# Optimization experiments

Measured on AMD Instinct MI355X. Metric: run time of the kernel, lower is better.

Reference implementation:

```python
import jax, jax.numpy as jnp
import numpy as np
import math

B = 256          # batch size
D = 128          # input_size (embed dim)
N = 500000       # output_size == num_samples (memory bank rows)
K = 2048         # num_negative_samples
T = 0.07         # temperature
MOM = 0.5        # momentum
EPS = 1e-07


def _l2norm(x):
    return x / jnp.linalg.norm(x, axis=-1, keepdims=True)


def setup_inputs() -> dict:
    key = jax.random.key(0)
    k1, k2, k3, k4, k5, k6 = jax.random.split(key, 6)
    stdv = 1.0 / math.sqrt(D / 3.0)
    memory_v1 = jax.random.uniform(k1, (N, D), dtype=jnp.float32) * (2 * stdv) - stdv
    memory_v2 = jax.random.uniform(k2, (N, D), dtype=jnp.float32) * (2 * stdv) - stdv
    # embeds come out of an L2-normalization module in the original pipeline
    student_embed = _l2norm(jax.random.normal(k3, (B, D), dtype=jnp.float32))
    teacher_embed = _l2norm(jax.random.normal(k4, (B, D), dtype=jnp.float32))
    pos_idx = jax.random.randint(k5, (B,), 0, N, dtype=jnp.int64)
    contrast_idx = jax.random.randint(k6, (B, K + 1), 0, N, dtype=jnp.int64)
    contrast_idx = contrast_idx.at[:, 0].set(pos_idx)  # column 0 holds the positive
    return {
        'student_embed': student_embed,
        'teacher_embed': teacher_embed,
        'memory_v1': memory_v1,
        'memory_v2': memory_v2,
        'pos_idx': pos_idx,
        'contrast_idx': contrast_idx,
    }


def _contrast_loss(x):
    # x: [B, K+1] normalized exp-similarities; column 0 is the positive
    m = x.shape[1] - 1
    pn = 1.0 / float(N)  # num_samples
    noise = m * pn + EPS
    p_pos = x[:, 0]
    log_d1 = jnp.log(p_pos / (p_pos + noise))
    p_neg = x[:, 1:]
    log_d0 = jnp.log((m * pn) / (p_neg + noise))
    return -(log_d1.sum() + log_d0.sum()) / x.shape[0]


def reference(student_embed, teacher_embed, memory_v1, memory_v2, pos_idx, contrast_idx):
    output_size = memory_v1.shape[0]
    # gather [B, K+1, D] rows from each bank (detached in original)
    w1 = jax.lax.stop_gradient(memory_v1[contrast_idx])
    w2 = jax.lax.stop_gradient(memory_v2[contrast_idx])
    # per-sample bmm + exp/div  (teacher scored against v1 bank, student against v2)
    out_v2 = jnp.exp(jnp.einsum('bkd,bd->bk', w1, teacher_embed) / T)
    out_v1 = jnp.exp(jnp.einsum('bkd,bd->bk', w2, student_embed) / T)
    # first-call normalization constants (treated as constants thereafter)
    z_v1 = jax.lax.stop_gradient(out_v1.mean() * output_size)
    z_v2 = jax.lax.stop_gradient(out_v2.mean() * output_size)
    out_v1 = out_v1 / z_v1
    out_v2 = out_v2 / z_v2
    # momentum-weighted renormalize-and-scatter memory update (no_grad)
    s = jax.lax.stop_gradient(student_embed)
    t = jax.lax.stop_gradient(teacher_embed)
    l_pos = memory_v1[pos_idx] * MOM + s * (1.0 - MOM)
    updated_v1 = l_pos / jnp.sqrt((l_pos ** 2).sum(1, keepdims=True))
    new_memory_v1 = memory_v1.at[pos_idx].set(updated_v1)
    ab_pos = memory_v2[pos_idx] * MOM + t * (1.0 - MOM)
    updated_v2 = ab_pos / jnp.sqrt((ab_pos ** 2).sum(1, keepdims=True))
    new_memory_v2 = memory_v2.at[pos_idx].set(updated_v2)
    loss = _contrast_loss(out_v1) + _contrast_loss(out_v2)
    return loss, new_memory_v1, new_memory_v2
```

## Files before the change

kernel.cpp:

```cpp
#include <hip/hip_runtime.h>
#include <math.h>

namespace {
constexpr int kB = 256;
constexpr int kD = 128;
constexpr int kN = 500000;
constexpr int kKC = 2049;
constexpr int kNPair = kB * kKC;
constexpr float kTInv = 1.0f / 0.07f;
constexpr float kMom = 0.5f;
constexpr int kRB = 256;
constexpr long long kM = (long long)kN * kD;
constexpr long long kTot = 2 * kM;
constexpr int kChunk = 2048;
constexpr int kNB1 = (kN + kChunk - 1) / kChunk;
constexpr int kRows = 32;
constexpr int kTPB = kN / kRows;
constexpr int kTiles = 2 * kTPB;
constexpr int kLdsStride = 132;
constexpr int kTilesPerBlock = 16;
constexpr int kGrid9 = (kTiles + kTilesPerBlock - 1) / kTilesPerBlock;

typedef float fx4 __attribute__((ext_vector_type(4)));
}


__global__ __launch_bounds__(256) void hist_kernel(const int* __restrict__ cidx, int* __restrict__ A)
{
    int i = blockIdx.x * 256 + threadIdx.x;
    if (i < kNPair) atomicAdd(&A[cidx[i]], 1);
}

__global__ __launch_bounds__(256) void scan1_kernel(const int* __restrict__ A, int* __restrict__ bsum)
{
    long long base = (long long)blockIdx.x * kChunk;
    int t = threadIdx.x;
    int s = 0;
    #pragma unroll
    for (int j = 0; j < 8; ++j) {
        long long i = base + t * 8 + j;
        if (i < kN) s += A[i];
    }
    __shared__ int lds[256];
    lds[t] = s; __syncthreads();
    for (int st = 128; st > 0; st >>= 1) {
        if (t < st) lds[t] += lds[t + st];
        __syncthreads();
    }
    if (t == 0) bsum[blockIdx.x] = lds[0];
}

__global__ __launch_bounds__(256) void scan2_kernel(
    const int* __restrict__ bsum, int* __restrict__ bpre, int* __restrict__ offs)
{
    int t = threadIdx.x;
    int v = (t < kNB1) ? bsum[t] : 0;
    __shared__ int lds[256];
    lds[t] = v; __syncthreads();
    for (int st = 1; st < 256; st <<= 1) {
        int add = (t >= st) ? lds[t - st] : 0;
        __syncthreads();
        lds[t] += add;
        __syncthreads();
    }
    if (t < kNB1) bpre[t] = lds[t] - v;
    if (t == kNB1 - 1) offs[kN] = lds[t];
}

__global__ __launch_bounds__(256) void scan3_kernel(
    const int* __restrict__ A, const int* __restrict__ bpre, int* __restrict__ offs)
{
    int t = threadIdx.x;
    long long base = (long long)blockIdx.x * kChunk;
    int c[8]; int s = 0;
    #pragma unroll
    for (int j = 0; j < 8; ++j) {
        long long i = base + t * 8 + j;
        c[j] = (i < kN) ? A[i] : 0;
        s += c[j];
    }
    __shared__ int lds[256];
    lds[t] = s; __syncthreads();
    for (int st = 1; st < 256; st <<= 1) {
        int add = (t >= st) ? lds[t - st] : 0;
        __syncthreads();
        lds[t] += add;
        __syncthreads();
    }
    int excl = lds[t] - s + bpre[blockIdx.x];
    #pragma unroll
    for (int j = 0; j < 8; ++j) {
        long long i = base + t * 8 + j;
        if (i < kN) { offs[i] = excl; excl += c[j]; }
    }
}

__global__ __launch_bounds__(256) void scatter_kernel(
    const int* __restrict__ cidx, const int* __restrict__ offs,
    int* __restrict__ cur, long long* __restrict__ sorted64)
{
    int p = blockIdx.x * 256 + threadIdx.x;
    if (p < kNPair) {
        int r = cidx[p];
        int pos = offs[r] + atomicAdd(&cur[r], 1);
        sorted64[pos] = ((long long)r << 20) | (long long)p;
    }
}

__global__ __launch_bounds__(256) void fused9_kernel(
    const float* __restrict__ mem1, const float* __restrict__ mem2,
    const float* __restrict__ teacher, const float* __restrict__ student,
    const int* __restrict__ offs, const long long* __restrict__ sorted64,
    float* __restrict__ out, float* __restrict__ e2, float* __restrict__ e1)
{
    __shared__ float tile[kRows * kLdsStride];
    __shared__ long long s64lds[2][256];
    const int tid = threadIdx.x;
    const int lane = tid & 63;
    const int w = tid >> 6;
    fx4* ov = reinterpret_cast<fx4*>(out);

    if (blockIdx.x == 0 && tid == 0)
        __builtin_nontemporal_store(mem2[kM - 1], &out[kTot]);

    const int T0 = blockIdx.x * kTilesPerBlock;
    int T1 = T0 + kTilesPerBlock; if (T1 > kTiles) T1 = kTiles;
    const int nT = T1 - T0;

    auto r0of = [](int T) { return (T >= kTPB) ? (T - kTPB) * kRows : T * kRows; };

    int rA = r0of(T0);
    int oA = offs[rA];
    int cA = offs[rA + kRows] - oA;
    int TBn = (1 < nT) ? T0 + 1 : T0;
    int rB = r0of(TBn);
    int oB = offs[rB];
    int cB = (1 < nT) ? (offs[rB + kRows] - oB) : 0;
    {
        long long v = 0;
        if (tid < cA) v = sorted64[oA + tid];
        s64lds[0][tid] = v;
    }
    float4 sl0, sl1, sl2, sl3;
    float carry;
    {
        int bk = (T0 >= kTPB);
        const float4* bank4 = reinterpret_cast<const float4*>(bk ? mem2 : mem1);
        long long lb4 = (long long)(bk ? T0 - kTPB : T0) * (kRows * kD / 4) + w * 256;
        sl0 = bank4[lb4 + 0 * 64 + lane];
        sl1 = bank4[lb4 + 1 * 64 + lane];
        sl2 = bank4[lb4 + 2 * 64 + lane];
        sl3 = bank4[lb4 + 3 * 64 + lane];
        long long gb = (long long)bk * kM + (long long)rA * kD + (long long)w * 1024;
        carry = 0.f;
        if (gb > 0) { long long g2 = gb - 1; carry = (g2 < kM) ? mem1[g2] : mem2[g2 - kM]; }
    }

    for (int i = 0; i < nT; ++i) {
        const int T = T0 + i;
        const int cur = i & 1;
        const int bk = (T >= kTPB) ? 1 : 0;
        const int r0 = r0of(T);
        const int o0 = oA, cnt = cA;

        float4 sn0, sn1, sn2, sn3;
        float carryn;
        {
            int Tn = (i + 1 < nT) ? T + 1 : T;
            int bkn = (Tn >= kTPB);
            const float4* bank4 = reinterpret_cast<const float4*>(bkn ? mem2 : mem1);
            long long lb4 = (long long)(bkn ? Tn - kTPB : Tn) * (kRows * kD / 4) + w * 256;
            sn0 = bank4[lb4 + 0 * 64 + lane];
            sn1 = bank4[lb4 + 1 * 64 + lane];
            sn2 = bank4[lb4 + 2 * 64 + lane];
            sn3 = bank4[lb4 + 3 * 64 + lane];
            long long gb = (long long)bkn * kM + (long long)r0of(Tn) * kD + (long long)w * 1024;
            carryn = 0.f;
            if (gb > 0) { long long g2 = gb - 1; carryn = (g2 < kM) ? mem1[g2] : mem2[g2 - kM]; }
        }
        long long s64n = 0;
        if (tid < cB) s64n = sorted64[oB + tid];
        int oC, cC;
        {
            int Tn2 = (i + 2 < nT) ? T + 2 : T;
            int rn2 = r0of(Tn2);
            oC = offs[rn2];
            cC = (i + 2 < nT) ? (offs[rn2 + kRows] - oC) : 0;
        }
        __builtin_amdgcn_sched_barrier(0);

        {
            const long long gbase = (long long)bk * kM + (long long)r0 * kD
                                    + (long long)w * 1024;
            const long long g4 = gbase >> 2;
            float cr = carry;
            float4 v[4] = {sl0, sl1, sl2, sl3};
            #pragma unroll
            for (int i2 = 0; i2 < 4; ++i2) {
                float4 c = v[i2];
                int lr = w * 8 + i2 * 2 + (lane >> 5);
                *reinterpret_cast<float4*>(&tile[lr * kLdsStride + (lane & 31) * 4]) = c;
                float pw = __shfl_up(c.w, 1);
                if (lane == 0) pw = cr;
                cr = __shfl(c.w, 63);
                long long k4 = g4 + i2 * 64 + lane;
                if (k4 != 0) {
                    fx4 st = {pw, c.x, c.y, c.z};
                    __builtin_nontemporal_store(st, &ov[k4]);
                } else {
                    __builtin_nontemporal_store(c.x, &out[1]);
                    __builtin_nontemporal_store(c.y, &out[2]);
                    __builtin_nontemporal_store(c.z, &out[3]);
                }
            }
        }
        asm volatile("s_waitcnt lgkmcnt(0)" ::: "memory");
        __builtin_amdgcn_sched_barrier(0);
        __builtin_amdgcn_s_barrier();
        __builtin_amdgcn_sched_barrier(0);

        {
            s64lds[cur ^ 1][tid] = s64n;

            const float4* emb4 = reinterpret_cast<const float4*>(bk ? student : teacher);
            float* ep = bk ? e1 : e2;
            const int sub = tid & 3;
            for (int t = tid >> 2; t < cnt; t += 64) {
                long long v = (t < 256) ? s64lds[cur][t] : sorted64[o0 + t];
                int p  = (int)(v & 0xFFFFF);
                int lr = (int)(v >> 20) - r0;
                const float4* er = emb4
                    + (long long)((unsigned)p / (unsigned)kKC) * 32 + sub * 8;
                const float* row = &tile[lr * kLdsStride + sub * 32];
                float ax = 0.f, ay = 0.f, az = 0.f, aw = 0.f;
                #pragma unroll
                for (int kk = 0; kk < 8; ++kk) {
                    int c4 = (kk + sub * 2) & 7;
                    float4 ev = er[c4];
                    float4 rv = *reinterpret_cast<const float4*>(&row[c4 * 4]);
                    ax += rv.x * ev.x; ay += rv.y * ev.y;
                    az += rv.z * ev.z; aw += rv.w * ev.w;
                }
                float d = (ax + ay) + (az + aw);
                d += __shfl_xor(d, 1);
                d += __shfl_xor(d, 2);
                if (sub == 0) ep[p] = __expf(d * kTInv);
            }
        }
        __builtin_amdgcn_sched_barrier(0);
        asm volatile("s_waitcnt lgkmcnt(0)" ::: "memory");
        __builtin_amdgcn_s_barrier();
        __builtin_amdgcn_sched_barrier(0);

        sl0 = sn0; sl1 = sn1; sl2 = sn2; sl3 = sn3;
        carry = carryn;
        oA = oB; cA = cB; oB = oC; cB = cC;
    }
}


__global__ __launch_bounds__(256) void dots_kernel(
    const float* __restrict__ mem1, const float* __restrict__ mem2,
    const float* __restrict__ teacher, const float* __restrict__ student,
    const int* __restrict__ cidx,
    float* __restrict__ e2, float* __restrict__ e1)
{
    int gtid = blockIdx.x * 256 + threadIdx.x;
    int wave = gtid >> 6;
    int lane = threadIdx.x & 63;
    if (wave >= kNPair) return;
    int b = wave / kKC;
    long long row = (long long)cidx[wave] * kD;
    const float2 m1 = *reinterpret_cast<const float2*>(mem1 + row + lane * 2);
    const float2 m2 = *reinterpret_cast<const float2*>(mem2 + row + lane * 2);
    const float2 tv = *reinterpret_cast<const float2*>(teacher + b * kD + lane * 2);
    const float2 sv = *reinterpret_cast<const float2*>(student + b * kD + lane * 2);
    float d1 = m1.x * tv.x + m1.y * tv.y;
    float d2 = m2.x * sv.x + m2.y * sv.y;
    #pragma unroll
    for (int off = 32; off > 0; off >>= 1) {
        d1 += __shfl_xor(d1, off);
        d2 += __shfl_xor(d2, off);
    }
    if (lane == 0) {
        e2[wave] = __expf(d1 * kTInv);
        e1[wave] = __expf(d2 * kTInv);
    }
}

__global__ __launch_bounds__(256) void copy_kernel(
    const float* __restrict__ mem1, const float* __restrict__ mem2,
    float* __restrict__ out)
{
    const long long NV4 = (kTot + 1) / 4;
    const long long KS  = kM / 4;
    const float4* m1v = reinterpret_cast<const float4*>(mem1);
    const float4* m2v = reinterpret_cast<const float4*>(mem2);
    float4* ov = reinterpret_cast<float4*>(out);
    long long stride = (long long)gridDim.x * 256;
    for (long long k = (long long)blockIdx.x * 256 + threadIdx.x; k < NV4; k += stride) {
        if (k == 0) {
            out[1] = mem1[0]; out[2] = mem1[1]; out[3] = mem1[2];
            out[kTot] = mem2[kM - 1];
            continue;
        }
        float4 r;
        if (k < KS) {
            float4 a = m1v[k - 1];
            float4 b = m1v[k];
            r = make_float4(a.w, b.x, b.y, b.z);
        } else if (k == KS) {
            r = make_float4(mem1[kM - 1], mem2[0], mem2[1], mem2[2]);
        } else {
            float4 a = m2v[k - KS - 1];
            float4 b = m2v[k - KS];
            r = make_float4(a.w, b.x, b.y, b.z);
        }
        ov[k] = r;
    }
}


__global__ __launch_bounds__(256) void sums_kernel(
    const float* __restrict__ e2, const float* __restrict__ e1,
    float* __restrict__ p2, float* __restrict__ p1)
{
    __shared__ float s2[256], s1[256];
    float a2 = 0.f, a1 = 0.f;
    for (int i = blockIdx.x * 256 + threadIdx.x; i < kNPair; i += 256 * kRB) {
        a2 += e2[i];
        a1 += e1[i];
    }
    s2[threadIdx.x] = a2; s1[threadIdx.x] = a1;
    __syncthreads();
    for (int st = 128; st > 0; st >>= 1) {
        if ((int)threadIdx.x < st) {
            s2[threadIdx.x] += s2[threadIdx.x + st];
            s1[threadIdx.x] += s1[threadIdx.x + st];
        }
        __syncthreads();
    }
    if (threadIdx.x == 0) { p2[blockIdx.x] = s2[0]; p1[blockIdx.x] = s1[0]; }
}

__global__ __launch_bounds__(256) void lossp_kernel(
    const float* __restrict__ e2, const float* __restrict__ e1,
    const float* __restrict__ p2, const float* __restrict__ p1,
    float* __restrict__ lp)
{
    __shared__ float s2[256], s1[256];
    s2[threadIdx.x] = p2[threadIdx.x];
    s1[threadIdx.x] = p1[threadIdx.x];
    __syncthreads();
    for (int st = 128; st > 0; st >>= 1) {
        if ((int)threadIdx.x < st) {
            s2[threadIdx.x] += s2[threadIdx.x + st];
            s1[threadIdx.x] += s1[threadIdx.x + st];
        }
        __syncthreads();
    }
    const float scale = (float)kN / (float)kNPair;
    const float iz2 = 1.0f / (s2[0] * scale);
    const float iz1 = 1.0f / (s1[0] * scale);

    const float mpn = 2048.0f / 500000.0f;
    const float noise = mpn + 1e-7f;
    float acc = 0.f;
    for (int i = blockIdx.x * 256 + threadIdx.x; i < kNPair; i += 256 * kRB) {
        int k = i % kKC;
        float x2 = e2[i] * iz2;
        float x1 = e1[i] * iz1;
        if (k == 0) {
            acc += __logf(x2 / (x2 + noise)) + __logf(x1 / (x1 + noise));
        } else {
            acc += __logf(mpn / (x2 + noise)) + __logf(mpn / (x1 + noise));
        }
    }
    __syncthreads();
    __shared__ float s[256];
    s[threadIdx.x] = acc;
    __syncthreads();
    for (int st = 128; st > 0; st >>= 1) {
        if ((int)threadIdx.x < st) s[threadIdx.x] += s[threadIdx.x + st];
        __syncthreads();
    }
    if (threadIdx.x == 0) lp[blockIdx.x] = s[0];
}

__global__ __launch_bounds__(256) void final_kernel(
    const float* __restrict__ lp, float* __restrict__ out)
{
    __shared__ float s[256];
    s[threadIdx.x] = lp[threadIdx.x];
    __syncthreads();
    for (int st = 128; st > 0; st >>= 1) {
        if ((int)threadIdx.x < st) s[threadIdx.x] += s[threadIdx.x + st];
        __syncthreads();
    }
    if (threadIdx.x == 0) out[0] = -s[0] / (float)kB;
}


__global__ __launch_bounds__(64) void update_kernel(
    const float* __restrict__ mem1, const float* __restrict__ mem2,
    const float* __restrict__ student, const float* __restrict__ teacher,
    const int* __restrict__ pos_idx,
    float* __restrict__ out1, float* __restrict__ out2)
{
    int b = blockIdx.x;
    int lane = threadIdx.x;
    int p = pos_idx[b];
    for (int b2 = b + 1; b2 < kB; ++b2)
        if (pos_idx[b2] == p) return;
    long long row = (long long)p * kD;
    float2 m1 = *reinterpret_cast<const float2*>(mem1 + row + lane * 2);
    float2 m2 = *reinterpret_cast<const float2*>(mem2 + row + lane * 2);
    float2 sv = *reinterpret_cast<const float2*>(student + b * kD + lane * 2);
    float2 tv = *reinterpret_cast<const float2*>(teacher + b * kD + lane * 2);
    float2 l1 = make_float2(m1.x * kMom + sv.x * (1.f - kMom),
                            m1.y * kMom + sv.y * (1.f - kMom));
    float2 l2 = make_float2(m2.x * kMom + tv.x * (1.f - kMom),
                            m2.y * kMom + tv.y * (1.f - kMom));
    float n1 = l1.x * l1.x + l1.y * l1.y;
    float n2 = l2.x * l2.x + l2.y * l2.y;
    #pragma unroll
    for (int off = 32; off > 0; off >>= 1) {
        n1 += __shfl_xor(n1, off);
        n2 += __shfl_xor(n2, off);
    }
    float i1 = 1.0f / sqrtf(n1);
    float i2 = 1.0f / sqrtf(n2);
    out1[row + lane * 2]     = l1.x * i1;
    out1[row + lane * 2 + 1] = l1.y * i1;
    out2[row + lane * 2]     = l2.x * i2;
    out2[row + lane * 2 + 1] = l2.y * i2;
}

extern "C" void kernel_launch(void* const* d_in, const int* in_sizes, int n_in,
                              void* d_out, int out_size, void* d_ws, size_t ws_size,
                              hipStream_t stream) {
    const float* student = (const float*)d_in[0];
    const float* teacher = (const float*)d_in[1];
    const float* mem1    = (const float*)d_in[2];
    const float* mem2    = (const float*)d_in[3];
    const int*   pos_idx = (const int*)d_in[4];
    const int*   cidx    = (const int*)d_in[5];

    float* out  = (float*)d_out;
    float* out1 = out + 1;
    float* out2 = out + 1 + kM;

    float* ws = (float*)d_ws;
    float* e2 = ws;
    float* e1 = e2 + kNPair;
    long long* sorted64 = (long long*)(e1 + kNPair);
    float* p2 = (float*)(sorted64 + kNPair);
    float* p1 = p2 + kRB;
    float* lp = p1 + kRB;
    int*   A    = (int*)(lp + kRB);
    int*   cur  = A + kN;
    int*   offs = cur + kN;
    int*   bsum = offs + kN + 1;
    int*   bpre = bsum + kNB1;
    size_t need = (size_t)((char*)(bpre + kNB1) - (char*)d_ws);

    if (ws_size >= need) {
        (void)hipMemsetAsync(A, 0, 2 * (size_t)kN * sizeof(int), stream);
        hist_kernel<<<(kNPair + 255) / 256, 256, 0, stream>>>(cidx, A);
        scan1_kernel<<<kNB1, 256, 0, stream>>>(A, bsum);
        scan2_kernel<<<1, 256, 0, stream>>>(bsum, bpre, offs);
        scan3_kernel<<<kNB1, 256, 0, stream>>>(A, bpre, offs);
        scatter_kernel<<<(kNPair + 255) / 256, 256, 0, stream>>>(cidx, offs, cur, sorted64);
        fused9_kernel<<<kGrid9, 256, 0, stream>>>(mem1, mem2, teacher, student,
                                                  offs, sorted64, out, e2, e1);
    } else {
        int nblocks = (kNPair + 3) / 4;
        dots_kernel<<<nblocks, 256, 0, stream>>>(mem1, mem2, teacher, student, cidx, e2, e1);
        copy_kernel<<<2048, 256, 0, stream>>>(mem1, mem2, out);
    }

    sums_kernel<<<kRB, 256, 0, stream>>>(e2, e1, p2, p1);
    lossp_kernel<<<kRB, 256, 0, stream>>>(e2, e1, p2, p1, lp);
    final_kernel<<<1, 256, 0, stream>>>(lp, out);
    update_kernel<<<kB, 64, 0, stream>>>(mem1, mem2, student, teacher, pos_idx, out1, out2);
}
```

Baseline: 309.1 us.

## Fuse exp-sum reduction into fused gather kernel and halve tiles per block

Each fused9 block now accumulates the exp-similarities it produces and writes per-block partial sums, so the separate sums pass that re-read both e arrays is removed. lossp then reduces the per-block partials itself. Tiles per block drop from 16 to 8 for more blocks, the staged index buffer shrinks to 128 entries, and the memset is replaced by a zeroing kernel. The trade-offs are more partials to reduce, an extra reduction tail in every fused block, and more global reads of sorted indices when a tile has more than 128 pairs.

```diff
diff --git a/kernel.cpp b/kernel.cpp
--- a/kernel.cpp
+++ b/kernel.cpp
@@ -18,12 +18,18 @@
 constexpr int kTPB = kN / kRows;
 constexpr int kTiles = 2 * kTPB;
 constexpr int kLdsStride = 132;
-constexpr int kTilesPerBlock = 16;
+constexpr int kTilesPerBlock = 8;
 constexpr int kGrid9 = (kTiles + kTilesPerBlock - 1) / kTilesPerBlock;
 
 typedef float fx4 __attribute__((ext_vector_type(4)));
 }
 
+
+__global__ __launch_bounds__(256) void zero2_kernel(int* __restrict__ A, int* __restrict__ cur)
+{
+    int i = blockIdx.x * 256 + threadIdx.x;
+    if (i < kN) { A[i] = 0; cur[i] = 0; }
+}
 
 __global__ __launch_bounds__(256) void hist_kernel(const int* __restrict__ cidx, int* __restrict__ A)
 {
@@ -111,14 +117,16 @@
     const float* __restrict__ mem1, const float* __restrict__ mem2,
     const float* __restrict__ teacher, const float* __restrict__ student,
     const int* __restrict__ offs, const long long* __restrict__ sorted64,
-    float* __restrict__ out, float* __restrict__ e2, float* __restrict__ e1)
+    float* __restrict__ out, float* __restrict__ e2, float* __restrict__ e1,
+    float* __restrict__ p2g, float* __restrict__ p1g)
 {
     __shared__ float tile[kRows * kLdsStride];
-    __shared__ long long s64lds[2][256];
+    __shared__ long long s64lds[2][128];
     const int tid = threadIdx.x;
     const int lane = tid & 63;
     const int w = tid >> 6;
     fx4* ov = reinterpret_cast<fx4*>(out);
+    float accE2 = 0.f, accE1 = 0.f;
 
     if (blockIdx.x == 0 && tid == 0)
         __builtin_nontemporal_store(mem2[kM - 1], &out[kTot]);
@@ -136,7 +144,7 @@
     int rB = r0of(TBn);
     int oB = offs[rB];
     int cB = (1 < nT) ? (offs[rB + kRows] - oB) : 0;
-    {
+    if (tid < 128) {
         long long v = 0;
         if (tid < cA) v = sorted64[oA + tid];
         s64lds[0][tid] = v;
@@ -179,7 +187,7 @@
             if (gb > 0) { long long g2 = gb - 1; carryn = (g2 < kM) ? mem1[g2] : mem2[g2 - kM]; }
         }
         long long s64n = 0;
-        if (tid < cB) s64n = sorted64[oB + tid];
+        if (tid < 128 && tid < cB) s64n = sorted64[oB + tid];
         int oC, cC;
         {
             int Tn2 = (i + 2 < nT) ? T + 2 : T;
@@ -220,13 +228,13 @@
         __builtin_amdgcn_sched_barrier(0);
 
         {
-            s64lds[cur ^ 1][tid] = s64n;
+            if (tid < 128) s64lds[cur ^ 1][tid] = s64n;
 
             const float4* emb4 = reinterpret_cast<const float4*>(bk ? student : teacher);
             float* ep = bk ? e1 : e2;
             const int sub = tid & 3;
             for (int t = tid >> 2; t < cnt; t += 64) {
-                long long v = (t < 256) ? s64lds[cur][t] : sorted64[o0 + t];
+                long long v = (t < 128) ? s64lds[cur][t] : sorted64[o0 + t];
                 int p  = (int)(v & 0xFFFFF);
                 int lr = (int)(v >> 20) - r0;
                 const float4* er = emb4
@@ -244,7 +252,11 @@
                 float d = (ax + ay) + (az + aw);
                 d += __shfl_xor(d, 1);
                 d += __shfl_xor(d, 2);
-                if (sub == 0) ep[p] = __expf(d * kTInv);
+                if (sub == 0) {
+                    float E = __expf(d * kTInv);
+                    ep[p] = E;
+                    if (bk) accE1 += E; else accE2 += E;
+                }
             }
         }
         __builtin_amdgcn_sched_barrier(0);
@@ -256,6 +268,24 @@
         carry = carryn;
         oA = oB; cA = cB; oB = oC; cB = cC;
     }
+
+    __syncthreads();
+    float* red = tile;
+    red[tid] = accE2;
+    __syncthreads();
+    for (int st = 128; st > 0; st >>= 1) {
+        if (tid < st) red[tid] += red[tid + st];
+        __syncthreads();
+    }
+    float s2v = red[0];
+    __syncthreads();
+    red[tid] = accE1;
+    __syncthreads();
+    for (int st = 128; st > 0; st >>= 1) {
+        if (tid < st) red[tid] += red[tid + st];
+        __syncthreads();
+    }
+    if (tid == 0) { p2g[blockIdx.x] = s2v; p1g[blockIdx.x] = red[0]; }
 }
 
 
@@ -320,7 +350,6 @@
     }
 }
 
-
 __global__ __launch_bounds__(256) void sums_kernel(
     const float* __restrict__ e2, const float* __restrict__ e1,
     float* __restrict__ p2, float* __restrict__ p1)
@@ -346,11 +375,13 @@
 __global__ __launch_bounds__(256) void lossp_kernel(
     const float* __restrict__ e2, const float* __restrict__ e1,
     const float* __restrict__ p2, const float* __restrict__ p1,
-    float* __restrict__ lp)
+    int np, float* __restrict__ lp)
 {
     __shared__ float s2[256], s1[256];
-    s2[threadIdx.x] = p2[threadIdx.x];
-    s1[threadIdx.x] = p1[threadIdx.x];
+    float a2 = 0.f, a1 = 0.f;
+    for (int i = threadIdx.x; i < np; i += 256) { a2 += p2[i]; a1 += p1[i]; }
+    s2[threadIdx.x] = a2;
+    s1[threadIdx.x] = a1;
     __syncthreads();
     for (int st = 128; st > 0; st >>= 1) {
         if ((int)threadIdx.x < st) {
@@ -454,9 +485,9 @@
     float* e2 = ws;
     float* e1 = e2 + kNPair;
     long long* sorted64 = (long long*)(e1 + kNPair);
-    float* p2 = (float*)(sorted64 + kNPair);
-    float* p1 = p2 + kRB;
-    float* lp = p1 + kRB;
+    float* p2g = (float*)(sorted64 + kNPair);
+    float* p1g = p2g + kGrid9;
+    float* lp  = p1g + kGrid9;
     int*   A    = (int*)(lp + kRB);
     int*   cur  = A + kN;
     int*   offs = cur + kN;
@@ -465,22 +496,24 @@
     size_t need = (size_t)((char*)(bpre + kNB1) - (char*)d_ws);
 
     if (ws_size >= need) {
-        (void)hipMemsetAsync(A, 0, 2 * (size_t)kN * sizeof(int), stream);
+        zero2_kernel<<<(kN + 255) / 256, 256, 0, stream>>>(A, cur);
         hist_kernel<<<(kNPair + 255) / 256, 256, 0, stream>>>(cidx, A);
         scan1_kernel<<<kNB1, 256, 0, stream>>>(A, bsum);
         scan2_kernel<<<1, 256, 0, stream>>>(bsum, bpre, offs);
         scan3_kernel<<<kNB1, 256, 0, stream>>>(A, bpre, offs);
         scatter_kernel<<<(kNPair + 255) / 256, 256, 0, stream>>>(cidx, offs, cur, sorted64);
         fused9_kernel<<<kGrid9, 256, 0, stream>>>(mem1, mem2, teacher, student,
-                                                  offs, sorted64, out, e2, e1);
+                                                  offs, sorted64, out, e2, e1,
+                                                  p2g, p1g);
+        lossp_kernel<<<kRB, 256, 0, stream>>>(e2, e1, p2g, p1g, kGrid9, lp);
     } else {
         int nblocks = (kNPair + 3) / 4;
         dots_kernel<<<nblocks, 256, 0, stream>>>(mem1, mem2, teacher, student, cidx, e2, e1);
         copy_kernel<<<2048, 256, 0, stream>>>(mem1, mem2, out);
-    }
-
-    sums_kernel<<<kRB, 256, 0, stream>>>(e2, e1, p2, p1);
-    lossp_kernel<<<kRB, 256, 0, stream>>>(e2, e1, p2, p1, lp);
+        sums_kernel<<<kRB, 256, 0, stream>>>(e2, e1, p2g, p1g);
+        lossp_kernel<<<kRB, 256, 0, stream>>>(e2, e1, p2g, p1g, kRB, lp);
+    }
+
     final_kernel<<<1, 256, 0, stream>>>(lp, out);
     update_kernel<<<kB, 64, 0, stream>>>(mem1, mem2, student, teacher, pos_idx, out1, out2);
 }
```

Measured after the change: 312.5 us. About the same (+1.1%).
